# Optimization experiments

Hardware: AMD Instinct MI355X
Metric: run time of the kernel (lower is better)

Reference implementation:

```python
import jax, jax.numpy as jnp
import numpy as np

N = 50000
E = 800000
IN_CH = 128
HID = 16
HEADS = 8
OUT_CH = 64
NEG_SLOPE = 0.2


def setup_inputs() -> dict:
    key = jax.random.key(0)
    ks = jax.random.split(key, 16)
    x = jax.random.normal(ks[0], (N, IN_CH), dtype=jnp.float32)
    edge_index = jax.random.randint(ks[1], (2, E), 0, N, dtype=jnp.int64)
    s = 0.05
    # GATv2 layer 1: in=128 -> heads=8, out=16 (concat -> 128)
    W1l = jax.random.normal(ks[2], (IN_CH, HEADS * HID), dtype=jnp.float32) * s
    b1l = jnp.zeros((HEADS * HID,), dtype=jnp.float32)
    W1r = jax.random.normal(ks[3], (IN_CH, HEADS * HID), dtype=jnp.float32) * s
    b1r = jnp.zeros((HEADS * HID,), dtype=jnp.float32)
    att1 = jax.random.normal(ks[4], (HEADS, HID), dtype=jnp.float32) * s
    bias1 = jnp.zeros((HEADS * HID,), dtype=jnp.float32)
    # GATv2 layer 2: in=128 -> heads=1, out=64
    W2l = jax.random.normal(ks[5], (HEADS * HID, OUT_CH), dtype=jnp.float32) * s
    b2l = jnp.zeros((OUT_CH,), dtype=jnp.float32)
    W2r = jax.random.normal(ks[6], (HEADS * HID, OUT_CH), dtype=jnp.float32) * s
    b2r = jnp.zeros((OUT_CH,), dtype=jnp.float32)
    att2 = jax.random.normal(ks[7], (1, OUT_CH), dtype=jnp.float32) * s
    bias2 = jnp.zeros((OUT_CH,), dtype=jnp.float32)
    return dict(x=x, edge_index=edge_index,
                W1l=W1l, b1l=b1l, W1r=W1r, b1r=b1r, att1=att1, bias1=bias1,
                W2l=W2l, b2l=b2l, W2r=W2r, b2r=b2r, att2=att2, bias2=bias2)


def gatv2_conv(x, src, dst, Wl, bl, Wr, br, att, bias, heads, out_ch, concat):
    n = x.shape[0]
    xl = (x @ Wl + bl).reshape(n, heads, out_ch)  # source transform
    xr = (x @ Wr + br).reshape(n, heads, out_ch)  # target transform
    m = xl[src] + xr[dst]                          # [E, H, C]
    m = jnp.where(m > 0, m, NEG_SLOPE * m)         # LeakyReLU(0.2)
    alpha = jnp.einsum('ehc,hc->eh', m, att)       # [E, H]
    # segment softmax over destination nodes (every node has a self loop)
    amax = jax.ops.segment_max(alpha, dst, num_segments=n)
    ea = jnp.exp(alpha - amax[dst])
    denom = jax.ops.segment_sum(ea, dst, num_segments=n)
    w = ea / denom[dst]                            # [E, H]
    out = jax.ops.segment_sum(xl[src] * w[:, :, None], dst, num_segments=n)
    if concat:
        out = out.reshape(n, heads * out_ch)
    else:
        out = out.mean(axis=1)
    return out + bias


def reference(x, edge_index, W1l, b1l, W1r, b1r, att1, bias1,
              W2l, b2l, W2r, b2r, att2, bias2):
    n = x.shape[0]
    loops = jnp.arange(n, dtype=edge_index.dtype)
    src = jnp.concatenate([edge_index[0], loops])
    dst = jnp.concatenate([edge_index[1], loops])
    # dropout layers are identity in eval mode
    h = gatv2_conv(x, src, dst, W1l, b1l, W1r, b1r, att1, bias1,
                   heads=HEADS, out_ch=HID, concat=True)
    h = jax.nn.elu(h)
    out = gatv2_conv(h, src, dst, W2l, b2l, W2r, b2r, att2, bias2,
                     heads=1, out_ch=OUT_CH, concat=True)
    return out
```

## Files before the change

### kernel.cpp

```cpp
#include <hip/hip_runtime.h>
#include <hip/hip_bf16.h>

constexpr int N_  = 50000;
constexpr int E_  = 800000;
constexpr int ET_ = 850000;
constexpr float NEG_SLOPE = 0.2f;

constexpr int SCAN_NB = (N_ + 255) / 256;
constexpr int CSR_CAP = 1250008;
constexpr int HT      = ET_ / 8;
constexpr int HB      = (HT + 255) / 256;
constexpr int G1B     = N_ / 16;
constexpr int ZERO4   = (50000 + CSR_CAP) / 4;

typedef __attribute__((ext_vector_type(8))) short short8;
typedef __attribute__((ext_vector_type(4))) float f32x4;

__device__ inline float leaky(float v) { return fmaxf(v, NEG_SLOPE * v); }

__device__ inline unsigned bf16rn(float f) {
    union { float f; unsigned u; } v; v.f = f;
    return (v.u + 0x7fffu + ((v.u >> 16) & 1u)) >> 16;
}
__device__ inline float2 unpack2(unsigned u) {
    return make_float2(__uint_as_float(u << 16), __uint_as_float(u & 0xffff0000u));
}

__device__ inline int edge_dst(int e, const int* __restrict__ ei) {
    return (e < E_) ? ei[E_ + e] : e - E_;
}
__device__ inline int edge_src(int e, const int* __restrict__ ei) {
    return (e < E_) ? ei[e] : e - E_;
}

__global__ __launch_bounds__(256) void init_kernel(
        const float* __restrict__ W1l, const float* __restrict__ W1r,
        const float* __restrict__ W2l, const float* __restrict__ W2r,
        unsigned short* __restrict__ wsw, unsigned short* __restrict__ wsw2,
        int4* __restrict__ zbase) {
    int gid = blockIdx.x * 256 + threadIdx.x;
    if (gid < ZERO4) zbase[gid] = make_int4(0, 0, 0, 0);
    if (gid < 32768) {
        int j    = gid & 7;
        int lane = (gid >> 3) & 63;
        int ks   = (gid >> 9) & 3;
        int ct   = gid >> 11;
        int k = ks * 32 + ((lane >> 4) & 3) * 8 + j;
        int c = ct * 16 + (lane & 15);
        float v = (c < 128) ? W1l[k * 128 + c] : W1r[k * 128 + (c - 128)];
        wsw[gid] = (unsigned short)bf16rn(v);
    } else if (gid < 49152) {
        int t2   = gid - 32768;
        int j    = t2 & 7;
        int lane = (t2 >> 3) & 63;
        int ks   = (t2 >> 9) & 3;
        int ct   = t2 >> 11;
        int k = ks * 32 + ((lane >> 4) & 3) * 8 + j;
        int c = ct * 16 + (lane & 15);
        float v = (c < 64) ? W2l[k * 64 + c] : W2r[k * 64 + (c - 64)];
        wsw2[t2] = (unsigned short)bf16rn(v);
    }
}

__global__ __launch_bounds__(256) void hist_gemm1(
        const int* __restrict__ ei, int* __restrict__ count, int* __restrict__ off,
        const float* __restrict__ x, const unsigned short* __restrict__ wsw,
        const float* __restrict__ bl, const float* __restrict__ br,
        unsigned short* __restrict__ xlu, float* __restrict__ xr1) {
    if (blockIdx.x < HB) {
        int t = blockIdx.x * 256 + threadIdx.x;
        if (t >= HT) return;
        int e8 = t * 8;
        int d[8], o[8];
        #pragma unroll
        for (int i = 0; i < 8; ++i) d[i] = edge_dst(e8 + i, ei);
        #pragma unroll
        for (int i = 0; i < 8; ++i) o[i] = atomicAdd(&count[d[i]], 1);
        int4* op = (int4*)(off + e8);
        op[0] = make_int4(o[0], o[1], o[2], o[3]);
        op[1] = make_int4(o[4], o[5], o[6], o[7]);
        return;
    }
    const int blk  = blockIdx.x - HB;
    const int wave = threadIdx.x >> 6;
    const int lane = threadIdx.x & 63;
    const int n0 = blk * 16;
    const int m = lane & 15;
    const int q = (lane >> 4) & 3;
    const float* __restrict__ arow = x + (size_t)(n0 + m) * 128 + q * 8;
    short8 afrag[4];
    #pragma unroll
    for (int ks = 0; ks < 4; ++ks) {
        float4 v0 = *(const float4*)(arow + ks * 32);
        float4 v1 = *(const float4*)(arow + ks * 32 + 4);
        short8 a;
        a[0] = (short)bf16rn(v0.x); a[1] = (short)bf16rn(v0.y);
        a[2] = (short)bf16rn(v0.z); a[3] = (short)bf16rn(v0.w);
        a[4] = (short)bf16rn(v1.x); a[5] = (short)bf16rn(v1.y);
        a[6] = (short)bf16rn(v1.z); a[7] = (short)bf16rn(v1.w);
        afrag[ks] = a;
    }
    #pragma unroll
    for (int i = 0; i < 4; ++i) {
        const int ct = wave * 4 + i;
        f32x4 acc = {0.f, 0.f, 0.f, 0.f};
        #pragma unroll
        for (int ks = 0; ks < 4; ++ks) {
            short8 b = *(const short8*)(wsw + ((size_t)(ct * 4 + ks) * 64 + lane) * 8);
            acc = __builtin_amdgcn_mfma_f32_16x16x32_bf16(afrag[ks], b, acc, 0, 0, 0);
        }
        const int col = ct * 16 + m;
        if (ct < 8) {
            float bias = bl[col];
            #pragma unroll
            for (int j = 0; j < 4; ++j) {
                int row = n0 + q * 4 + j;
                xlu[(size_t)row * 128 + col] = (unsigned short)bf16rn(acc[j] + bias);
            }
        } else {
            float bias = br[col - 128];
            #pragma unroll
            for (int j = 0; j < 4; ++j) {
                int row = n0 + q * 4 + j;
                xr1[(size_t)row * 128 + (col - 128)] = acc[j] + bias;
            }
        }
    }
}

__global__ __launch_bounds__(256) void scan_partial(
        const int* __restrict__ count, int* __restrict__ bsum) {
    __shared__ int red[256];
    int t = threadIdx.x;
    int i = blockIdx.x * 256 + t;
    red[t] = (i < N_) ? ((count[i] + 7) & ~7) : 0;
    __syncthreads();
    #pragma unroll
    for (int o = 128; o > 0; o >>= 1) {
        if (t < o) red[t] += red[t + o];
        __syncthreads();
    }
    if (t == 0) bsum[blockIdx.x] = red[0];
}

__global__ __launch_bounds__(256) void scan_final2(
        const int* __restrict__ count, const int* __restrict__ bsum,
        int* __restrict__ start) {
    __shared__ int top[256];
    __shared__ int buf[256];
    int t = threadIdx.x;
    top[t] = (t < SCAN_NB) ? bsum[t] : 0;
    __syncthreads();
    #pragma unroll
    for (int o = 1; o < 256; o <<= 1) {
        int add = (t >= o) ? top[t - o] : 0;
        __syncthreads();
        top[t] += add;
        __syncthreads();
    }
    int bst = (blockIdx.x == 0) ? 0 : top[blockIdx.x - 1];
    int i = blockIdx.x * 256 + t;
    int v = (i < N_) ? ((count[i] + 7) & ~7) : 0;
    buf[t] = v;
    __syncthreads();
    #pragma unroll
    for (int o = 1; o < 256; o <<= 1) {
        int add = (t >= o) ? buf[t - o] : 0;
        __syncthreads();
        buf[t] += add;
        __syncthreads();
    }
    if (i < N_) start[i] = bst + buf[t] - v;
}

__global__ __launch_bounds__(256) void scatter_kernel(
        const int* __restrict__ ei, const int* __restrict__ start,
        const int* __restrict__ off, int* __restrict__ csr_src) {
    int t = blockIdx.x * 256 + threadIdx.x;
    if (t >= HT) return;
    int e8 = t * 8;
    int4 o0 = *(const int4*)(off + e8);
    int4 o1 = *(const int4*)(off + e8 + 4);
    int o[8] = {o0.x, o0.y, o0.z, o0.w, o1.x, o1.y, o1.z, o1.w};
    int s[8], d[8];
    #pragma unroll
    for (int i = 0; i < 8; ++i) {
        s[i] = edge_src(e8 + i, ei);
        d[i] = edge_dst(e8 + i, ei);
    }
    int st[8];
    #pragma unroll
    for (int i = 0; i < 8; ++i) st[i] = start[d[i]];
    #pragma unroll
    for (int i = 0; i < 8; ++i) csr_src[st[i] + o[i]] = s[i];
}

__global__ __launch_bounds__(256) void fused1(
        const int* __restrict__ csr_src, const int* __restrict__ start,
        const int* __restrict__ count,
        const unsigned* __restrict__ xl1b, const float* __restrict__ xr1,
        const float* __restrict__ att, const float* __restrict__ bias1,
        float* __restrict__ hout) {
    int t = blockIdx.x * 256 + threadIdx.x;
    int n = __builtin_amdgcn_readfirstlane(t >> 6);
    int lane = t & 63;
    if (n >= N_) return;
    float2 xr = *(const float2*)(xr1 + (size_t)n * 128 + 2 * lane);
    float2 av = *(const float2*)(att + 2 * lane);
    int p0 = __builtin_amdgcn_readfirstlane(start[n]);
    int p1 = p0 + __builtin_amdgcn_readfirstlane(count[n]);
    float2 acc = make_float2(0.f, 0.f);
    float l = 0.f;
    for (int p = p0; p < p1; p += 4) {
        int4 si = *(const int4*)(csr_src + p);
        int s0 = __builtin_amdgcn_readfirstlane(si.x);
        int s1 = __builtin_amdgcn_readfirstlane(si.y);
        int s2 = __builtin_amdgcn_readfirstlane(si.z);
        int s3 = __builtin_amdgcn_readfirstlane(si.w);
        float2 x0 = unpack2(xl1b[(size_t)s0 * 64 + lane]);
        float2 x1 = unpack2(xl1b[(size_t)s1 * 64 + lane]);
        float2 x2 = unpack2(xl1b[(size_t)s2 * 64 + lane]);
        float2 x3 = unpack2(xl1b[(size_t)s3 * 64 + lane]);
        float a0 = fmaf(leaky(x0.x + xr.x), av.x, leaky(x0.y + xr.y) * av.y);
        float a1 = fmaf(leaky(x1.x + xr.x), av.x, leaky(x1.y + xr.y) * av.y);
        float a2 = fmaf(leaky(x2.x + xr.x), av.x, leaky(x2.y + xr.y) * av.y);
        float a3 = fmaf(leaky(x3.x + xr.x), av.x, leaky(x3.y + xr.y) * av.y);
        a0 += __shfl_xor(a0, 1); a1 += __shfl_xor(a1, 1);
        a2 += __shfl_xor(a2, 1); a3 += __shfl_xor(a3, 1);
        a0 += __shfl_xor(a0, 2); a1 += __shfl_xor(a1, 2);
        a2 += __shfl_xor(a2, 2); a3 += __shfl_xor(a3, 2);
        a0 += __shfl_xor(a0, 4); a1 += __shfl_xor(a1, 4);
        a2 += __shfl_xor(a2, 4); a3 += __shfl_xor(a3, 4);
        float w0 = __expf(a0);
        float w1 = p + 1 < p1 ? __expf(a1) : 0.f;
        float w2 = p + 2 < p1 ? __expf(a2) : 0.f;
        float w3 = p + 3 < p1 ? __expf(a3) : 0.f;
        acc.x = fmaf(w0, x0.x, acc.x); acc.y = fmaf(w0, x0.y, acc.y); l += w0;
        acc.x = fmaf(w1, x1.x, acc.x); acc.y = fmaf(w1, x1.y, acc.y); l += w1;
        acc.x = fmaf(w2, x2.x, acc.x); acc.y = fmaf(w2, x2.y, acc.y); l += w2;
        acc.x = fmaf(w3, x3.x, acc.x); acc.y = fmaf(w3, x3.y, acc.y); l += w3;
    }
    float2 bv = *(const float2*)(bias1 + 2 * lane);
    float vx = acc.x / l + bv.x;
    float vy = acc.y / l + bv.y;
    float2 o;
    o.x = vx > 0.f ? vx : (__expf(vx) - 1.f);
    o.y = vy > 0.f ? vy : (__expf(vy) - 1.f);
    *(float2*)(hout + (size_t)n * 128 + 2 * lane) = o;
}

__global__ __launch_bounds__(256) void gemm2_mfma(
        const float* __restrict__ hbuf,
        const unsigned short* __restrict__ wsw2,
        const float* __restrict__ bl, const float* __restrict__ br,
        unsigned short* __restrict__ xlu2, float* __restrict__ xr2) {
    const int wave = threadIdx.x >> 6;
    const int lane = threadIdx.x & 63;
    const int n0 = blockIdx.x * 16;
    const int m = lane & 15;
    const int q = (lane >> 4) & 3;
    const float* __restrict__ arow = hbuf + (size_t)(n0 + m) * 128 + q * 8;
    short8 afrag[4];
    #pragma unroll
    for (int ks = 0; ks < 4; ++ks) {
        float4 v0 = *(const float4*)(arow + ks * 32);
        float4 v1 = *(const float4*)(arow + ks * 32 + 4);
        short8 a;
        a[0] = (short)bf16rn(v0.x); a[1] = (short)bf16rn(v0.y);
        a[2] = (short)bf16rn(v0.z); a[3] = (short)bf16rn(v0.w);
        a[4] = (short)bf16rn(v1.x); a[5] = (short)bf16rn(v1.y);
        a[6] = (short)bf16rn(v1.z); a[7] = (short)bf16rn(v1.w);
        afrag[ks] = a;
    }
    #pragma unroll
    for (int i = 0; i < 2; ++i) {
        const int ct = wave * 2 + i;
        f32x4 acc = {0.f, 0.f, 0.f, 0.f};
        #pragma unroll
        for (int ks = 0; ks < 4; ++ks) {
            short8 b = *(const short8*)(wsw2 + ((size_t)(ct * 4 + ks) * 64 + lane) * 8);
            acc = __builtin_amdgcn_mfma_f32_16x16x32_bf16(afrag[ks], b, acc, 0, 0, 0);
        }
        const int col = ct * 16 + m;
        if (ct < 4) {
            float bias = bl[col];
            #pragma unroll
            for (int j = 0; j < 4; ++j) {
                int row = n0 + q * 4 + j;
                xlu2[(size_t)row * 64 + col] = (unsigned short)bf16rn(acc[j] + bias);
            }
        } else {
            float bias = br[col - 64];
            #pragma unroll
            for (int j = 0; j < 4; ++j) {
                int row = n0 + q * 4 + j;
                xr2[(size_t)row * 64 + (col - 64)] = acc[j] + bias;
            }
        }
    }
}

__global__ __launch_bounds__(256) void fused2(
        const int* __restrict__ csr_src, const int* __restrict__ start,
        const int* __restrict__ count,
        const unsigned* __restrict__ xl2b, const float* __restrict__ xr2,
        const float* __restrict__ att, const float* __restrict__ bias2,
        float* __restrict__ out) {
    int t = blockIdx.x * 256 + threadIdx.x;
    int n = __builtin_amdgcn_readfirstlane(t >> 6);
    int lane = t & 63;
    int half = lane >> 5;
    int lc   = lane & 31;
    if (n >= N_) return;
    float2 xr = *(const float2*)(xr2 + (size_t)n * 64 + 2 * lc);
    float2 av = *(const float2*)(att + 2 * lc);
    int p0 = __builtin_amdgcn_readfirstlane(start[n]);
    int p1 = p0 + __builtin_amdgcn_readfirstlane(count[n]);
    float2 acc = make_float2(0.f, 0.f);
    float l = 0.f;
    for (int p = p0; p < p1; p += 8) {
        int4 ia = *(const int4*)(csr_src + p);
        int4 ib = *(const int4*)(csr_src + p + 4);
        int sx[8];
        sx[0] = __builtin_amdgcn_readfirstlane(ia.x);
        sx[1] = __builtin_amdgcn_readfirstlane(ia.y);
        sx[2] = __builtin_amdgcn_readfirstlane(ia.z);
        sx[3] = __builtin_amdgcn_readfirstlane(ia.w);
        sx[4] = __builtin_amdgcn_readfirstlane(ib.x);
        sx[5] = __builtin_amdgcn_readfirstlane(ib.y);
        sx[6] = __builtin_amdgcn_readfirstlane(ib.z);
        sx[7] = __builtin_amdgcn_readfirstlane(ib.w);
        #pragma unroll
        for (int u = 0; u < 4; ++u) {
            int pe = p + 2 * u + half;
            int s  = sx[2 * u + half];
            float2 xv = unpack2(xl2b[(size_t)s * 32 + lc]);
            float a = fmaf(leaky(xv.x + xr.x), av.x, leaky(xv.y + xr.y) * av.y);
            a += __shfl_xor(a, 1);
            a += __shfl_xor(a, 2);
            a += __shfl_xor(a, 4);
            a += __shfl_xor(a, 8);
            a += __shfl_xor(a, 16);
            float w = pe < p1 ? __expf(a) : 0.f;
            acc.x = fmaf(w, xv.x, acc.x);
            acc.y = fmaf(w, xv.y, acc.y);
            l += w;
        }
    }
    acc.x += __shfl_xor(acc.x, 32);
    acc.y += __shfl_xor(acc.y, 32);
    l     += __shfl_xor(l, 32);
    if (half == 0) {
        float2 bv = *(const float2*)(bias2 + 2 * lc);
        float2 o;
        o.x = acc.x / l + bv.x;
        o.y = acc.y / l + bv.y;
        *(float2*)(out + (size_t)n * 64 + 2 * lc) = o;
    }
}

extern "C" void kernel_launch(void* const* d_in, const int* in_sizes, int n_in,
                              void* d_out, int out_size, void* d_ws, size_t ws_size,
                              hipStream_t stream) {
    (void)in_sizes; (void)n_in; (void)out_size; (void)ws_size;
    const float* x     = (const float*)d_in[0];
    const int*   ei    = (const int*)d_in[1];
    const float* W1l   = (const float*)d_in[2];
    const float* b1l   = (const float*)d_in[3];
    const float* W1r   = (const float*)d_in[4];
    const float* b1r   = (const float*)d_in[5];
    const float* att1  = (const float*)d_in[6];
    const float* bias1 = (const float*)d_in[7];
    const float* W2l   = (const float*)d_in[8];
    const float* b2l   = (const float*)d_in[9];
    const float* W2r   = (const float*)d_in[10];
    const float* b2r   = (const float*)d_in[11];
    const float* att2  = (const float*)d_in[12];
    const float* bias2 = (const float*)d_in[13];
    float* out = (float*)d_out;

    float* xr1      = (float*)d_ws;
    float* hbuf     = xr1 + 6400000;
    unsigned* xl1b  = (unsigned*)(hbuf + 6400000);
    int* count   = (int*)(xl1b + 3200000);
    int* csr_src = count + 50000;
    int* startp  = csr_src + CSR_CAP;
    int* off     = startp + 50000;
    int* bsum    = off + 850000;
    int* bstart  = bsum + 256;
    unsigned short* wsw2 = (unsigned short*)(bstart + 256);
    unsigned* xl2b = xl1b;
    float* xr2     = xr1;
    unsigned short* wsw = (unsigned short*)hbuf;

    init_kernel<<<(ZERO4 + 255) / 256, 256, 0, stream>>>(W1l, W1r, W2l, W2r,
                                                         wsw, wsw2, (int4*)count);
    hist_gemm1 <<<HB + G1B, 256, 0, stream>>>(ei, count, off, x, wsw, b1l, b1r,
                                              (unsigned short*)xl1b, xr1);
    scan_partial<<<SCAN_NB, 256, 0, stream>>>(count, bsum);
    scan_final2 <<<SCAN_NB, 256, 0, stream>>>(count, bsum, startp);
    scatter_kernel<<<(HT + 255) / 256, 256, 0, stream>>>(ei, startp, off, csr_src);

    fused1<<<(N_ * 64 + 255) / 256, 256, 0, stream>>>(csr_src, startp, count,
                                                      xl1b, xr1, att1, bias1, hbuf);
    gemm2_mfma <<<N_ / 16, 256, 0, stream>>>(hbuf, wsw2, b2l, b2r,
                                             (unsigned short*)xl2b, xr2);
    fused2<<<(N_ * 64 + 255) / 256, 256, 0, stream>>>(csr_src, startp, count,
                                                      xl2b, xr2, att2, bias2, out);
}
```

Baseline: 271.4 us.

## Build CSR with atomic cursors, move GEMM1 into scatter pass, stage GEMM outputs

The histogram pass now only counts degrees and no longer writes per-edge offsets. The scan also initialises a cursor array, and the scatter uses atomicAdd on that cursor to place sources. The layer-1 GEMM now runs in the same launch as the scatter instead of alongside the histogram. Both GEMM kernels stage their outputs through shared memory so global stores are row-contiguous. This removes the 850k-entry offset buffer's write and read and the start[] gather, at the cost of a second round of atomics. Ordering within each CSR segment becomes nondeterministic, which may slightly change float summation order.

```diff
diff --git a/kernel.cpp b/kernel.cpp
--- a/kernel.cpp
+++ b/kernel.cpp
@@ -24,13 +24,6 @@
 }
 __device__ inline float2 unpack2(unsigned u) {
     return make_float2(__uint_as_float(u << 16), __uint_as_float(u & 0xffff0000u));
-}
-
-__device__ inline int edge_dst(int e, const int* __restrict__ ei) {
-    return (e < E_) ? ei[E_ + e] : e - E_;
-}
-__device__ inline int edge_src(int e, const int* __restrict__ ei) {
-    return (e < E_) ? ei[e] : e - E_;
 }
 
 __global__ __launch_bounds__(256) void init_kernel(
@@ -62,23 +55,105 @@
     }
 }
 
-__global__ __launch_bounds__(256) void hist_gemm1(
-        const int* __restrict__ ei, int* __restrict__ count, int* __restrict__ off,
+__global__ __launch_bounds__(256) void hist_kernel(
+        const int* __restrict__ ei, int* __restrict__ count) {
+    int t = blockIdx.x * 256 + threadIdx.x;
+    if (t >= HT) return;
+    int e8 = t * 8;
+    int d[8];
+    if (e8 < E_) {
+        int4 a = *(const int4*)(ei + E_ + e8);
+        int4 b = *(const int4*)(ei + E_ + e8 + 4);
+        d[0] = a.x; d[1] = a.y; d[2] = a.z; d[3] = a.w;
+        d[4] = b.x; d[5] = b.y; d[6] = b.z; d[7] = b.w;
+    } else {
+        #pragma unroll
+        for (int i = 0; i < 8; ++i) d[i] = e8 + i - E_;
+    }
+    #pragma unroll
+    for (int i = 0; i < 8; ++i) atomicAdd(&count[d[i]], 1);
+}
+
+__global__ __launch_bounds__(256) void scan_partial(
+        const int* __restrict__ count, int* __restrict__ bsum) {
+    __shared__ int red[256];
+    int t = threadIdx.x;
+    int i = blockIdx.x * 256 + t;
+    red[t] = (i < N_) ? ((count[i] + 7) & ~7) : 0;
+    __syncthreads();
+    #pragma unroll
+    for (int o = 128; o > 0; o >>= 1) {
+        if (t < o) red[t] += red[t + o];
+        __syncthreads();
+    }
+    if (t == 0) bsum[blockIdx.x] = red[0];
+}
+
+__global__ __launch_bounds__(256) void scan_final2(
+        const int* __restrict__ count, const int* __restrict__ bsum,
+        int* __restrict__ start, int* __restrict__ cur) {
+    __shared__ int top[256];
+    __shared__ int buf[256];
+    int t = threadIdx.x;
+    top[t] = (t < SCAN_NB) ? bsum[t] : 0;
+    __syncthreads();
+    #pragma unroll
+    for (int o = 1; o < 256; o <<= 1) {
+        int add = (t >= o) ? top[t - o] : 0;
+        __syncthreads();
+        top[t] += add;
+        __syncthreads();
+    }
+    int bst = (blockIdx.x == 0) ? 0 : top[blockIdx.x - 1];
+    int i = blockIdx.x * 256 + t;
+    int v = (i < N_) ? ((count[i] + 7) & ~7) : 0;
+    buf[t] = v;
+    __syncthreads();
+    #pragma unroll
+    for (int o = 1; o < 256; o <<= 1) {
+        int add = (t >= o) ? buf[t - o] : 0;
+        __syncthreads();
+        buf[t] += add;
+        __syncthreads();
+    }
+    if (i < N_) {
+        int sv = bst + buf[t] - v;
+        start[i] = sv;
+        cur[i]   = sv;
+    }
+}
+
+__global__ __launch_bounds__(256) void scatter_gemm1(
+        const int* __restrict__ ei, int* __restrict__ cur,
+        int* __restrict__ csr_src,
         const float* __restrict__ x, const unsigned short* __restrict__ wsw,
         const float* __restrict__ bl, const float* __restrict__ br,
         unsigned short* __restrict__ xlu, float* __restrict__ xr1) {
+    __shared__ unsigned short lu[16][132];
+    __shared__ float          lr[16][132];
     if (blockIdx.x < HB) {
         int t = blockIdx.x * 256 + threadIdx.x;
         if (t >= HT) return;
         int e8 = t * 8;
-        int d[8], o[8];
-        #pragma unroll
-        for (int i = 0; i < 8; ++i) d[i] = edge_dst(e8 + i, ei);
-        #pragma unroll
-        for (int i = 0; i < 8; ++i) o[i] = atomicAdd(&count[d[i]], 1);
-        int4* op = (int4*)(off + e8);
-        op[0] = make_int4(o[0], o[1], o[2], o[3]);
-        op[1] = make_int4(o[4], o[5], o[6], o[7]);
+        int s[8], d[8];
+        if (e8 < E_) {
+            int4 sa = *(const int4*)(ei + e8);
+            int4 sb = *(const int4*)(ei + e8 + 4);
+            int4 da = *(const int4*)(ei + E_ + e8);
+            int4 db = *(const int4*)(ei + E_ + e8 + 4);
+            s[0] = sa.x; s[1] = sa.y; s[2] = sa.z; s[3] = sa.w;
+            s[4] = sb.x; s[5] = sb.y; s[6] = sb.z; s[7] = sb.w;
+            d[0] = da.x; d[1] = da.y; d[2] = da.z; d[3] = da.w;
+            d[4] = db.x; d[5] = db.y; d[6] = db.z; d[7] = db.w;
+        } else {
+            #pragma unroll
+            for (int i = 0; i < 8; ++i) { s[i] = e8 + i - E_; d[i] = s[i]; }
+        }
+        int o[8];
+        #pragma unroll
+        for (int i = 0; i < 8; ++i) o[i] = atomicAdd(&cur[d[i]], 1);
+        #pragma unroll
+        for (int i = 0; i < 8; ++i) csr_src[o[i]] = s[i];
         return;
     }
     const int blk  = blockIdx.x - HB;
@@ -109,90 +184,30 @@
             short8 b = *(const short8*)(wsw + ((size_t)(ct * 4 + ks) * 64 + lane) * 8);
             acc = __builtin_amdgcn_mfma_f32_16x16x32_bf16(afrag[ks], b, acc, 0, 0, 0);
         }
-        const int col = ct * 16 + m;
         if (ct < 8) {
+            const int col = ct * 16 + m;
             float bias = bl[col];
             #pragma unroll
-            for (int j = 0; j < 4; ++j) {
-                int row = n0 + q * 4 + j;
-                xlu[(size_t)row * 128 + col] = (unsigned short)bf16rn(acc[j] + bias);
-            }
+            for (int j = 0; j < 4; ++j)
+                lu[q * 4 + j][col] = (unsigned short)bf16rn(acc[j] + bias);
         } else {
-            float bias = br[col - 128];
+            const int col = (ct - 8) * 16 + m;
+            float bias = br[col];
             #pragma unroll
-            for (int j = 0; j < 4; ++j) {
-                int row = n0 + q * 4 + j;
-                xr1[(size_t)row * 128 + (col - 128)] = acc[j] + bias;
-            }
-        }
-    }
-}
-
-__global__ __launch_bounds__(256) void scan_partial(
-        const int* __restrict__ count, int* __restrict__ bsum) {
-    __shared__ int red[256];
-    int t = threadIdx.x;
-    int i = blockIdx.x * 256 + t;
-    red[t] = (i < N_) ? ((count[i] + 7) & ~7) : 0;
+            for (int j = 0; j < 4; ++j)
+                lr[q * 4 + j][col] = acc[j] + bias;
+        }
+    }
     __syncthreads();
-    #pragma unroll
-    for (int o = 128; o > 0; o >>= 1) {
-        if (t < o) red[t] += red[t + o];
-        __syncthreads();
-    }
-    if (t == 0) bsum[blockIdx.x] = red[0];
-}
-
-__global__ __launch_bounds__(256) void scan_final2(
-        const int* __restrict__ count, const int* __restrict__ bsum,
-        int* __restrict__ start) {
-    __shared__ int top[256];
-    __shared__ int buf[256];
-    int t = threadIdx.x;
-    top[t] = (t < SCAN_NB) ? bsum[t] : 0;
-    __syncthreads();
-    #pragma unroll
-    for (int o = 1; o < 256; o <<= 1) {
-        int add = (t >= o) ? top[t - o] : 0;
-        __syncthreads();
-        top[t] += add;
-        __syncthreads();
-    }
-    int bst = (blockIdx.x == 0) ? 0 : top[blockIdx.x - 1];
-    int i = blockIdx.x * 256 + t;
-    int v = (i < N_) ? ((count[i] + 7) & ~7) : 0;
-    buf[t] = v;
-    __syncthreads();
-    #pragma unroll
-    for (int o = 1; o < 256; o <<= 1) {
-        int add = (t >= o) ? buf[t - o] : 0;
-        __syncthreads();
-        buf[t] += add;
-        __syncthreads();
-    }
-    if (i < N_) start[i] = bst + buf[t] - v;
-}
-
-__global__ __launch_bounds__(256) void scatter_kernel(
-        const int* __restrict__ ei, const int* __restrict__ start,
-        const int* __restrict__ off, int* __restrict__ csr_src) {
-    int t = blockIdx.x * 256 + threadIdx.x;
-    if (t >= HT) return;
-    int e8 = t * 8;
-    int4 o0 = *(const int4*)(off + e8);
-    int4 o1 = *(const int4*)(off + e8 + 4);
-    int o[8] = {o0.x, o0.y, o0.z, o0.w, o1.x, o1.y, o1.z, o1.w};
-    int s[8], d[8];
-    #pragma unroll
-    for (int i = 0; i < 8; ++i) {
-        s[i] = edge_src(e8 + i, ei);
-        d[i] = edge_dst(e8 + i, ei);
-    }
-    int st[8];
-    #pragma unroll
-    for (int i = 0; i < 8; ++i) st[i] = start[d[i]];
-    #pragma unroll
-    for (int i = 0; i < 8; ++i) csr_src[st[i] + o[i]] = s[i];
+    unsigned* __restrict__ xlu32 = (unsigned*)xlu;
+    #pragma unroll
+    for (int k = 0; k < 4; ++k) {
+        int r = wave * 4 + k;
+        unsigned w = *(const unsigned*)&lu[r][2 * lane];
+        xlu32[(size_t)(n0 + r) * 64 + lane] = w;
+        float2 f = make_float2(lr[r][2 * lane], lr[r][2 * lane + 1]);
+        *(float2*)(xr1 + (size_t)(n0 + r) * 128 + 2 * lane) = f;
+    }
 }
 
 __global__ __launch_bounds__(256) void fused1(
@@ -254,6 +269,8 @@
         const unsigned short* __restrict__ wsw2,
         const float* __restrict__ bl, const float* __restrict__ br,
         unsigned short* __restrict__ xlu2, float* __restrict__ xr2) {
+    __shared__ unsigned short lu2[16][68];
+    __shared__ float          lr2[16][68];
     const int wave = threadIdx.x >> 6;
     const int lane = threadIdx.x & 63;
     const int n0 = blockIdx.x * 16;
@@ -281,22 +298,33 @@
             short8 b = *(const short8*)(wsw2 + ((size_t)(ct * 4 + ks) * 64 + lane) * 8);
             acc = __builtin_amdgcn_mfma_f32_16x16x32_bf16(afrag[ks], b, acc, 0, 0, 0);
         }
-        const int col = ct * 16 + m;
         if (ct < 4) {
+            const int col = ct * 16 + m;
             float bias = bl[col];
             #pragma unroll
-            for (int j = 0; j < 4; ++j) {
-                int row = n0 + q * 4 + j;
-                xlu2[(size_t)row * 64 + col] = (unsigned short)bf16rn(acc[j] + bias);
-            }
+            for (int j = 0; j < 4; ++j)
+                lu2[q * 4 + j][col] = (unsigned short)bf16rn(acc[j] + bias);
         } else {
-            float bias = br[col - 64];
+            const int col = (ct - 4) * 16 + m;
+            float bias = br[col];
             #pragma unroll
-            for (int j = 0; j < 4; ++j) {
-                int row = n0 + q * 4 + j;
-                xr2[(size_t)row * 64 + (col - 64)] = acc[j] + bias;
-            }
-        }
+            for (int j = 0; j < 4; ++j)
+                lr2[q * 4 + j][col] = acc[j] + bias;
+        }
+    }
+    __syncthreads();
+    unsigned* __restrict__ xlu232 = (unsigned*)xlu2;
+    #pragma unroll
+    for (int k = 0; k < 2; ++k) {
+        int rr = wave * 4 + 2 * k + (lane >> 5);
+        int c  = lane & 31;
+        unsigned w = *(const unsigned*)&lu2[rr][2 * c];
+        xlu232[(size_t)(n0 + rr) * 32 + c] = w;
+    }
+    #pragma unroll
+    for (int k = 0; k < 4; ++k) {
+        int r = wave * 4 + k;
+        xr2[(size_t)(n0 + r) * 64 + lane] = lr2[r][lane];
     }
 }
 
@@ -385,8 +413,8 @@
     int* count   = (int*)(xl1b + 3200000);
     int* csr_src = count + 50000;
     int* startp  = csr_src + CSR_CAP;
-    int* off     = startp + 50000;
-    int* bsum    = off + 850000;
+    int* cur     = startp + 50000;
+    int* bsum    = cur + 850000;
     int* bstart  = bsum + 256;
     unsigned short* wsw2 = (unsigned short*)(bstart + 256);
     unsigned* xl2b = xl1b;
@@ -395,12 +423,12 @@
 
     init_kernel<<<(ZERO4 + 255) / 256, 256, 0, stream>>>(W1l, W1r, W2l, W2r,
                                                          wsw, wsw2, (int4*)count);
-    hist_gemm1 <<<HB + G1B, 256, 0, stream>>>(ei, count, off, x, wsw, b1l, b1r,
-                                              (unsigned short*)xl1b, xr1);
+    hist_kernel<<<HB, 256, 0, stream>>>(ei, count);
     scan_partial<<<SCAN_NB, 256, 0, stream>>>(count, bsum);
-    scan_final2 <<<SCAN_NB, 256, 0, stream>>>(count, bsum, startp);
-    scatter_kernel<<<(HT + 255) / 256, 256, 0, stream>>>(ei, startp, off, csr_src);
-
+    scan_final2 <<<SCAN_NB, 256, 0, stream>>>(count, bsum, startp, cur);
+    scatter_gemm1<<<HB + G1B, 256, 0, stream>>>(ei, cur, csr_src, x, wsw,
+                                                b1l, b1r,
+                                                (unsigned short*)xl1b, xr1);
     fused1<<<(N_ * 64 + 255) / 256, 256, 0, stream>>>(csr_src, startp, count,
                                                       xl1b, xr1, att1, bias1, hbuf);
     gemm2_mfma <<<N_ / 16, 256, 0, stream>>>(hbuf, wsw2, b2l, b2r,
```

Result: slower. 293.9 us (+8.3%).
